# Optimization experiments

Hardware: AMD Instinct MI355X
Metric: run time of the kernel (lower is better)

Reference implementation:

```python
import jax, jax.numpy as jnp
import numpy as np

B, S, D = 16, 2048, 768
DOWNS = [16, 32, 64, 128]


def setup_inputs() -> dict:
    key = jax.random.key(0)
    ks = jax.random.split(key, 2 + 4 * len(DOWNS))
    inp = {
        "x": jax.random.normal(ks[0], (B, S, D), dtype=jnp.float32),
        "mask": jax.random.randint(ks[1], (B, S), 0, len(DOWNS), dtype=jnp.int64),
    }
    k = 2
    for i, ds in enumerate(DOWNS):
        inp[f"Wd{i}"] = jax.random.normal(ks[k], (D, ds), dtype=jnp.float32) * 0.02; k += 1
        inp[f"bd{i}"] = jax.random.normal(ks[k], (ds,), dtype=jnp.float32) * 0.02; k += 1
        inp[f"Wu{i}"] = jax.random.normal(ks[k], (ds, D), dtype=jnp.float32) * 0.02; k += 1
        inp[f"bu{i}"] = jax.random.normal(ks[k], (D,), dtype=jnp.float32) * 0.02; k += 1
    return inp


def reference(x, mask,
              Wd0, bd0, Wu0, bu0,
              Wd1, bd1, Wu1, bu1,
              Wd2, bd2, Wu2, bu2,
              Wd3, bd3, Wu3, bu3):
    # eval path, inference_level==0: all experts densely computed, then
    # per-token random mask selects one expert output (with residual) and sums.
    params = [(Wd0, bd0, Wu0, bu0), (Wd1, bd1, Wu1, bu1),
              (Wd2, bd2, Wu2, bu2), (Wd3, bd3, Wu3, bu3)]
    out = jnp.zeros_like(x)
    for i, (Wd, bd, Wu, bu) in enumerate(params):
        down = jax.nn.relu(jnp.einsum('bsd,dk->bsk', x, Wd) + bd)  # dropout is identity in eval
        up = jnp.einsum('bsk,kd->bsd', down, Wu) + bu + x          # residual add
        sel = (mask == i)[..., None].astype(x.dtype)               # [B,S,1]
        out = out + up * sel
    return out
```

## Files before the change

kernel.cpp:

```cpp
#include <hip/hip_runtime.h>
#include <hip/hip_bf16.h>

#define DIM 768
#define NTOK 32768
#define TTOK 16
#define NBLK 128
#define GRID_MAIN 1024

typedef __attribute__((ext_vector_type(8))) short short8;
typedef __attribute__((ext_vector_type(4))) float f32x4;

__device__ __forceinline__ unsigned short f2bf(float f) {
  union { float f; unsigned int u; } v; v.f = f;
  unsigned int u = v.u;
  return (unsigned short)((u + 0x7fffu + ((u >> 16) & 1u)) >> 16);
}
__device__ __forceinline__ float bf2f(unsigned short u) {
  union { unsigned int u; float f; } v; v.u = ((unsigned int)u) << 16; return v.f;
}

__global__ void hist_kernel(const int* __restrict__ mask, int* __restrict__ hist) {
  int tid = threadIdx.x, b = blockIdx.x;
  int gid = b * 256 + tid;
  int wv = tid >> 6, lane = tid & 63;
  int e = mask[gid] & 3;
  __shared__ int wcnt[4][4];
  #pragma unroll
  for (int q = 0; q < 4; ++q) {
    unsigned long long m = __ballot(e == q);
    if (lane == 0) wcnt[wv][q] = __popcll(m);
  }
  __syncthreads();
  if (tid < 4)
    hist[tid * NBLK + b] = wcnt[0][tid] + wcnt[1][tid] + wcnt[2][tid] + wcnt[3][tid];
}

__global__ void scan_kernel(const int* __restrict__ hist, int* __restrict__ base,
                            int* __restrict__ meta) {
  int lane = threadIdx.x;
  int v[8];
  int lsum = 0;
  #pragma unroll
  for (int j = 0; j < 8; ++j) {
    int t = hist[lane * 8 + j];
    v[j] = lsum; lsum += t;
  }
  int inc = lsum;
  #pragma unroll
  for (int d = 1; d < 64; d <<= 1) {
    int u = __shfl_up(inc, d);
    if (lane >= d) inc += u;
  }
  int excl = inc - lsum;
  #pragma unroll
  for (int j = 0; j < 8; ++j) base[lane * 8 + j] = excl + v[j];
  __syncthreads();
  if (lane == 0) {
    int est[5];
    #pragma unroll
    for (int e = 0; e < 4; ++e) est[e] = base[e * NBLK];
    est[4] = NTOK;
    int s = 0;
    #pragma unroll
    for (int e = 0; e < 5; ++e) meta[e] = est[e];
    #pragma unroll
    for (int e = 0; e < 4; ++e) {
      meta[8 + e] = s;
      s += (est[e + 1] - est[e] + TTOK - 1) / TTOK;
    }
    meta[12] = s;
  }
}

__global__ void scatter_kernel(const int* __restrict__ mask, const int* __restrict__ base,
                               int* __restrict__ lists) {
  int tid = threadIdx.x, b = blockIdx.x;
  int gid = b * 256 + tid;
  int wv = tid >> 6, lane = tid & 63;
  int e = mask[gid] & 3;
  __shared__ int wcnt[4][4];
  __shared__ int wbase[4][4];
  unsigned long long lt = (1ull << lane) - 1ull;
  int rank = 0;
  #pragma unroll
  for (int q = 0; q < 4; ++q) {
    unsigned long long m = __ballot(e == q);
    if (e == q) rank = __popcll(m & lt);
    if (lane == 0) wcnt[wv][q] = __popcll(m);
  }
  __syncthreads();
  if (tid < 4) {
    int s = 0;
    #pragma unroll
    for (int w2 = 0; w2 < 4; ++w2) { int c = wcnt[w2][tid]; wbase[w2][tid] = s; s += c; }
  }
  __syncthreads();
  lists[base[e * NBLK + b] + wbase[wv][e] + rank] = gid;
}

__global__ void prep_kernel(const float* __restrict__ Wd0, const float* __restrict__ Wd1,
                            const float* __restrict__ Wd2, const float* __restrict__ Wd3,
                            const float* __restrict__ Wu0, const float* __restrict__ Wu1,
                            const float* __restrict__ Wu2, const float* __restrict__ Wu3,
                            unsigned short* __restrict__ wdT, unsigned short* __restrict__ wuT) {
  int e = blockIdx.x;
  int ds = 16 << e;
  int lgK = (e == 0) ? 5 : (4 + e);
  int KP = 1 << lgK;
  const float* Wd = (e == 0) ? Wd0 : (e == 1) ? Wd1 : (e == 2) ? Wd2 : Wd3;
  const float* Wu = (e == 0) ? Wu0 : (e == 1) ? Wu1 : (e == 2) ? Wu2 : Wu3;
  const int WOFF[4] = {0, 12288, 36864, 86016};
  const int UOFF[4] = {0, 24576, 49152, 98304};
  int stride = gridDim.y * 256;
  int start = blockIdx.y * 256 + threadIdx.x;
  int nd = ds * DIM;
  for (int i = start; i < nd; i += stride) {
    int k = i / DIM, d = i - k * DIM;
    wdT[WOFF[e] + i] = f2bf(Wd[d * ds + k]);
  }
  int nu = DIM << lgK;
  for (int i = start; i < nu; i += stride) {
    int dc = i >> lgK, k = i & (KP - 1);
    wuT[UOFF[e] + i] = (k < ds) ? f2bf(Wu[k * DIM + dc]) : (unsigned short)0;
  }
}

struct Pref {
  float4 v[6];
  int tk[4];
};

__device__ __forceinline__ void issue_prefetch(
    int w, int wv, int lane,
    const int* __restrict__ meta, const int* __restrict__ lists,
    const float* __restrict__ x, Pref& p) {
  const int* ts = meta + 8;
  int e = (w >= ts[2]) ? ((w >= ts[3]) ? 3 : 2) : ((w >= ts[1]) ? 1 : 0);
  int base = (w - ts[e]) * TTOK;
  int cnt = meta[e + 1] - meta[e];
  const int* listsE = lists + meta[e];
  #pragma unroll
  for (int i = 0; i < 4; ++i) {
    int r = base + wv * 4 + i;
    p.tk[i] = (r < cnt) ? listsE[r] : -1;
  }
  #pragma unroll
  for (int i = 0; i < 2; ++i) {
    int t = p.tk[i];
    const float* src = x + (size_t)((t >= 0) ? t : 0) * DIM;
    #pragma unroll
    for (int j = 0; j < 3; ++j) {
      float4 vv = {0.f, 0.f, 0.f, 0.f};
      if (t >= 0) vv = *(const float4*)(src + j * 256 + lane * 4);
      p.v[i * 3 + j] = vv;
    }
  }
}

template <int E>
__device__ __forceinline__ void moe_tile(
    int wv, int lane, int tid,
    const float* __restrict__ x,
    const unsigned short* __restrict__ wdT, const unsigned short* __restrict__ wuT,
    const float* __restrict__ bd, const float* __restrict__ bu,
    float* __restrict__ out, const int mytk[4],
    unsigned short* xsol, float* dnpart, unsigned short (*dn)[136]) {
  constexpr int DS = 16 << E;
  constexpr int KP = (E == 0) ? 32 : DS;
  constexpr int NTA = DS / 16;
  constexpr int SPLIT_N = (NTA < 4) ? NTA : 4;
  constexpr int SPLIT_K = 4 / SPLIT_N;
  constexpr int NTB = NTA / SPLIT_N;
  constexpr int KLEN = DIM / SPLIT_K;
  constexpr int KB = KP / 32;
  constexpr int WOFF[4] = {0, 12288, 36864, 86016};
  constexpr int UOFF[4] = {0, 24576, 49152, 98304};
  const unsigned short* wd = wdT + WOFF[E];
  const unsigned short* wu = wuT + UOFF[E];
  #define XS(r) (xsol + (r) * 776)
  #define OL(r) (xsol + (r) * 772)

  int lrow = lane & 15, kg = lane >> 4;

  if (SPLIT_K > 1) {
    for (int i = tid; i < TTOK * DS; i += 256) dnpart[i] = 0.f;
  }
  __syncthreads();

  int nsub = wv % SPLIT_N, ksub = wv / SPLIT_N;
  int d_base = ksub * KLEN;

  f32x4 acc[NTB];
  #pragma unroll
  for (int nb = 0; nb < NTB; ++nb) acc[nb] = f32x4{0.f, 0.f, 0.f, 0.f};

  for (int d0 = 0; d0 < KLEN; d0 += 64) {
    #pragma unroll
    for (int u = 0; u < 2; ++u) {
      int d = d_base + d0 + u * 32;
      short8 a = *(const short8*)(XS(lrow) + d + kg * 8);
      #pragma unroll
      for (int nb = 0; nb < NTB; ++nb) {
        int n = nsub * NTB + nb;
        short8 b = *(const short8*)(wd + (size_t)(n * 16 + lrow) * DIM + d + kg * 8);
        acc[nb] = __builtin_amdgcn_mfma_f32_16x16x32_bf16(a, b, acc[nb], 0, 0, 0);
      }
    }
  }

  if (SPLIT_K > 1) {
    #pragma unroll
    for (int nb = 0; nb < NTB; ++nb) {
      int kc = (nsub * NTB + nb) * 16 + lrow;
      #pragma unroll
      for (int r = 0; r < 4; ++r)
        atomicAdd(&dnpart[(kg * 4 + r) * DS + kc], acc[nb][r]);
    }
    __syncthreads();
    for (int i = tid; i < TTOK * KP; i += 256) {
      int tt = i / KP, k = i - tt * KP;
      float v = (k < DS) ? fmaxf(dnpart[tt * DS + k] + bd[k], 0.f) : 0.f;
      dn[tt][k] = f2bf(v);
    }
  } else {
    #pragma unroll
    for (int nb = 0; nb < NTB; ++nb) {
      int kc = (nsub * NTB + nb) * 16 + lrow;
      float bv = bd[kc];
      #pragma unroll
      for (int r = 0; r < 4; ++r)
        dn[kg * 4 + r][kc] = f2bf(fmaxf(acc[nb][r] + bv, 0.f));
    }
  }
  __syncthreads();

  short8 afr[KB];
  #pragma unroll
  for (int k = 0; k < KB; ++k) afr[k] = *(const short8*)&dn[lrow][k * 32 + kg * 8];

  #pragma unroll 3
  for (int nn = 0; nn < 12; ++nn) {
    int n = wv * 12 + nn;
    f32x4 c = {0.f, 0.f, 0.f, 0.f};
    #pragma unroll
    for (int k = 0; k < KB; ++k) {
      short8 b = *(const short8*)(wu + (size_t)(n * 16 + lrow) * KP + k * 32 + kg * 8);
      c = __builtin_amdgcn_mfma_f32_16x16x32_bf16(afr[k], b, c, 0, 0, 0);
    }
    int dcol = n * 16 + lrow;
    float bv = bu[dcol];
    #pragma unroll
    for (int r = 0; r < 4; ++r)
      OL(kg * 4 + r)[dcol] = f2bf(c[r] + bv);
  }
  __syncthreads();

  #pragma unroll
  for (int i = 0; i < 4; ++i) {
    int r = wv * 4 + i;
    int t = mytk[i];
    if (t < 0) continue;
    const float* xsrc = x + (size_t)t * DIM;
    float* dst = out + (size_t)t * DIM;
    #pragma unroll
    for (int j = 0; j < 3; ++j) {
      int c = j * 256 + lane * 4;
      float4 xv = *(const float4*)(xsrc + c);
      ushort4 ub = *(const ushort4*)(OL(r) + c);
      float4 o;
      o.x = xv.x + bf2f(ub.x);
      o.y = xv.y + bf2f(ub.y);
      o.z = xv.z + bf2f(ub.z);
      o.w = xv.w + bf2f(ub.w);
      *(float4*)(dst + c) = o;
    }
  }
  __syncthreads();
  #undef XS
  #undef OL
}

__global__ __launch_bounds__(256, 4) void moe_main(
    const float* __restrict__ x,
    const int* __restrict__ meta, const int* __restrict__ lists,
    const unsigned short* __restrict__ wdT, const unsigned short* __restrict__ wuT,
    const float* __restrict__ bd0, const float* __restrict__ bd1,
    const float* __restrict__ bd2, const float* __restrict__ bd3,
    const float* __restrict__ bu0, const float* __restrict__ bu1,
    const float* __restrict__ bu2, const float* __restrict__ bu3,
    float* __restrict__ out) {
  __shared__ unsigned short xsol[TTOK * 776];
  __shared__ float dnpart[TTOK * 32];
  __shared__ unsigned short dn[TTOK][136];
  int tid = threadIdx.x, wv = tid >> 6, lane = tid & 63;
  const int* ts = meta + 8;
  int ntiles = ts[4];
  int w0 = blockIdx.x;
  if (w0 >= ntiles) return;

  Pref p;
  issue_prefetch(w0, wv, lane, meta, lists, x, p);

  for (int w = w0; w < ntiles; w += GRID_MAIN) {
    int t2 = p.tk[2], t3 = p.tk[3];
    float4 s[6];
    {
      const float* s2 = x + (size_t)((t2 >= 0) ? t2 : 0) * DIM;
      const float* s3 = x + (size_t)((t3 >= 0) ? t3 : 0) * DIM;
      #pragma unroll
      for (int j = 0; j < 3; ++j) {
        float4 a = {0.f, 0.f, 0.f, 0.f}, b = {0.f, 0.f, 0.f, 0.f};
        if (t2 >= 0) a = *(const float4*)(s2 + j * 256 + lane * 4);
        if (t3 >= 0) b = *(const float4*)(s3 + j * 256 + lane * 4);
        s[j] = a; s[3 + j] = b;
      }
    }
    #pragma unroll
    for (int i = 0; i < 2; ++i) {
      int r = wv * 4 + i;
      #pragma unroll
      for (int j = 0; j < 3; ++j) {
        float4 vv = p.v[i * 3 + j];
        ushort4 b;
        b.x = f2bf(vv.x); b.y = f2bf(vv.y); b.z = f2bf(vv.z); b.w = f2bf(vv.w);
        *(ushort4*)(xsol + r * 776 + j * 256 + lane * 4) = b;
      }
    }
    #pragma unroll
    for (int i = 0; i < 2; ++i) {
      int r = wv * 4 + 2 + i;
      #pragma unroll
      for (int j = 0; j < 3; ++j) {
        float4 vv = s[i * 3 + j];
        ushort4 b;
        b.x = f2bf(vv.x); b.y = f2bf(vv.y); b.z = f2bf(vv.z); b.w = f2bf(vv.w);
        *(ushort4*)(xsol + r * 776 + j * 256 + lane * 4) = b;
      }
    }
    int mytk[4];
    #pragma unroll
    for (int i = 0; i < 4; ++i) mytk[i] = p.tk[i];

    int wn = w + GRID_MAIN;
    if (wn < ntiles) issue_prefetch(wn, wv, lane, meta, lists, x, p);

    int e = (w >= ts[2]) ? ((w >= ts[3]) ? 3 : 2) : ((w >= ts[1]) ? 1 : 0);
    if (e == 0)
      moe_tile<0>(wv, lane, tid, x, wdT, wuT, bd0, bu0, out, mytk, xsol, dnpart, dn);
    else if (e == 1)
      moe_tile<1>(wv, lane, tid, x, wdT, wuT, bd1, bu1, out, mytk, xsol, dnpart, dn);
    else if (e == 2)
      moe_tile<2>(wv, lane, tid, x, wdT, wuT, bd2, bu2, out, mytk, xsol, dnpart, dn);
    else
      moe_tile<3>(wv, lane, tid, x, wdT, wuT, bd3, bu3, out, mytk, xsol, dnpart, dn);
  }
}

extern "C" void kernel_launch(void* const* d_in, const int* in_sizes, int n_in,
                              void* d_out, int out_size, void* d_ws, size_t ws_size,
                              hipStream_t stream) {
  const float* x = (const float*)d_in[0];
  const int* mask = (const int*)d_in[1];
  const float* Wd[4]; const float* bd[4]; const float* Wu[4]; const float* bu[4];
  for (int i = 0; i < 4; ++i) {
    Wd[i] = (const float*)d_in[2 + 4 * i];
    bd[i] = (const float*)d_in[3 + 4 * i];
    Wu[i] = (const float*)d_in[4 + 4 * i];
    bu[i] = (const float*)d_in[5 + 4 * i];
  }
  char* ws = (char*)d_ws;
  int* hist = (int*)ws;
  int* base = (int*)(ws + 2048);
  int* meta = (int*)(ws + 4096);
  int* lists = (int*)(ws + 4352);
  unsigned short* wdT = (unsigned short*)(ws + 135424);
  unsigned short* wuT = (unsigned short*)(ws + 504064);

  hist_kernel<<<NBLK, 256, 0, stream>>>(mask, hist);
  scan_kernel<<<1, 64, 0, stream>>>(hist, base, meta);
  scatter_kernel<<<NBLK, 256, 0, stream>>>(mask, base, lists);
  prep_kernel<<<dim3(4, 32), 256, 0, stream>>>(Wd[0], Wd[1], Wd[2], Wd[3],
                                               Wu[0], Wu[1], Wu[2], Wu[3], wdT, wuT);
  moe_main<<<GRID_MAIN, 256, 0, stream>>>(x, meta, lists, wdT, wuT,
                                          bd[0], bd[1], bd[2], bd[3],
                                          bu[0], bu[1], bu[2], bu[3],
                                          (float*)d_out);
}
```

Measured before the change: 96.68 us.

## Reuse LDS bf16 x copy for residual, prefetch all rows, stagger block starts

The residual add now reads the bf16 copy of x already staged in shared memory and fuses it into the up-projection epilogue. This removes the second global read of each x row in the output pass. The prefetch path now loads all four token rows for the next tile, and blocks are staggered with s_sleep by cohort. __syncthreads is replaced by an explicit lgkmcnt wait plus s_barrier. The cost is that the residual is now bf16-rounded and summed in bf16, which adds numerical error, and the larger prefetch needs more registers.

Result: no change. 96.83 us (+0.2%).

```diff
diff --git a/kernel.cpp b/kernel.cpp
--- a/kernel.cpp
+++ b/kernel.cpp
@@ -6,6 +6,7 @@
 #define TTOK 16
 #define NBLK 128
 #define GRID_MAIN 1024
+#define XP 772
 
 typedef __attribute__((ext_vector_type(8))) short short8;
 typedef __attribute__((ext_vector_type(4))) float f32x4;
@@ -17,6 +18,12 @@
 }
 __device__ __forceinline__ float bf2f(unsigned short u) {
   union { unsigned int u; float f; } v; v.u = ((unsigned int)u) << 16; return v.f;
+}
+
+__device__ __forceinline__ void barrier_lds() {
+  asm volatile("s_waitcnt lgkmcnt(0)" ::: "memory");
+  __builtin_amdgcn_s_barrier();
+  asm volatile("" ::: "memory");
 }
 
 __global__ void hist_kernel(const int* __restrict__ mask, int* __restrict__ hist) {
@@ -125,8 +132,12 @@
   }
 }
 
+__device__ __forceinline__ int expert_of(int w, const int* __restrict__ ts) {
+  return (w >= ts[2]) ? ((w >= ts[3]) ? 3 : 2) : ((w >= ts[1]) ? 1 : 0);
+}
+
 struct Pref {
-  float4 v[6];
+  float4 v[12];
   int tk[4];
 };
 
@@ -135,7 +146,7 @@
     const int* __restrict__ meta, const int* __restrict__ lists,
     const float* __restrict__ x, Pref& p) {
   const int* ts = meta + 8;
-  int e = (w >= ts[2]) ? ((w >= ts[3]) ? 3 : 2) : ((w >= ts[1]) ? 1 : 0);
+  int e = expert_of(w, ts);
   int base = (w - ts[e]) * TTOK;
   int cnt = meta[e + 1] - meta[e];
   const int* listsE = lists + meta[e];
@@ -145,7 +156,7 @@
     p.tk[i] = (r < cnt) ? listsE[r] : -1;
   }
   #pragma unroll
-  for (int i = 0; i < 2; ++i) {
+  for (int i = 0; i < 4; ++i) {
     int t = p.tk[i];
     const float* src = x + (size_t)((t >= 0) ? t : 0) * DIM;
     #pragma unroll
@@ -160,11 +171,11 @@
 template <int E>
 __device__ __forceinline__ void moe_tile(
     int wv, int lane, int tid,
-    const float* __restrict__ x,
     const unsigned short* __restrict__ wdT, const unsigned short* __restrict__ wuT,
     const float* __restrict__ bd, const float* __restrict__ bu,
     float* __restrict__ out, const int mytk[4],
-    unsigned short* xsol, float* dnpart, unsigned short (*dn)[136]) {
+    unsigned short* __restrict__ xsol, float* __restrict__ dnpart,
+    unsigned short (*dn)[136]) {
   constexpr int DS = 16 << E;
   constexpr int KP = (E == 0) ? 32 : DS;
   constexpr int NTA = DS / 16;
@@ -177,15 +188,13 @@
   constexpr int UOFF[4] = {0, 24576, 49152, 98304};
   const unsigned short* wd = wdT + WOFF[E];
   const unsigned short* wu = wuT + UOFF[E];
-  #define XS(r) (xsol + (r) * 776)
-  #define OL(r) (xsol + (r) * 772)
 
   int lrow = lane & 15, kg = lane >> 4;
 
   if (SPLIT_K > 1) {
     for (int i = tid; i < TTOK * DS; i += 256) dnpart[i] = 0.f;
   }
-  __syncthreads();
+  barrier_lds();
 
   int nsub = wv % SPLIT_N, ksub = wv / SPLIT_N;
   int d_base = ksub * KLEN;
@@ -198,7 +207,7 @@
     #pragma unroll
     for (int u = 0; u < 2; ++u) {
       int d = d_base + d0 + u * 32;
-      short8 a = *(const short8*)(XS(lrow) + d + kg * 8);
+      short8 a = *(const short8*)(xsol + lrow * XP + d + kg * 8);
       #pragma unroll
       for (int nb = 0; nb < NTB; ++nb) {
         int n = nsub * NTB + nb;
@@ -216,7 +225,7 @@
       for (int r = 0; r < 4; ++r)
         atomicAdd(&dnpart[(kg * 4 + r) * DS + kc], acc[nb][r]);
     }
-    __syncthreads();
+    barrier_lds();
     for (int i = tid; i < TTOK * KP; i += 256) {
       int tt = i / KP, k = i - tt * KP;
       float v = (k < DS) ? fmaxf(dnpart[tt * DS + k] + bd[k], 0.f) : 0.f;
@@ -232,7 +241,7 @@
         dn[kg * 4 + r][kc] = f2bf(fmaxf(acc[nb][r] + bv, 0.f));
     }
   }
-  __syncthreads();
+  barrier_lds();
 
   short8 afr[KB];
   #pragma unroll
@@ -250,34 +259,31 @@
     int dcol = n * 16 + lrow;
     float bv = bu[dcol];
     #pragma unroll
-    for (int r = 0; r < 4; ++r)
-      OL(kg * 4 + r)[dcol] = f2bf(c[r] + bv);
-  }
-  __syncthreads();
+    for (int r = 0; r < 4; ++r) {
+      int t = kg * 4 + r;
+      unsigned short* cell = xsol + t * XP + dcol;
+      float xr = bf2f(*cell);
+      *cell = f2bf(c[r] + bv + xr);
+    }
+  }
+  barrier_lds();
 
   #pragma unroll
   for (int i = 0; i < 4; ++i) {
     int r = wv * 4 + i;
     int t = mytk[i];
     if (t < 0) continue;
-    const float* xsrc = x + (size_t)t * DIM;
     float* dst = out + (size_t)t * DIM;
     #pragma unroll
     for (int j = 0; j < 3; ++j) {
       int c = j * 256 + lane * 4;
-      float4 xv = *(const float4*)(xsrc + c);
-      ushort4 ub = *(const ushort4*)(OL(r) + c);
+      ushort4 ub = *(const ushort4*)(xsol + r * XP + c);
       float4 o;
-      o.x = xv.x + bf2f(ub.x);
-      o.y = xv.y + bf2f(ub.y);
-      o.z = xv.z + bf2f(ub.z);
-      o.w = xv.w + bf2f(ub.w);
+      o.x = bf2f(ub.x); o.y = bf2f(ub.y); o.z = bf2f(ub.z); o.w = bf2f(ub.w);
       *(float4*)(dst + c) = o;
     }
   }
-  __syncthreads();
-  #undef XS
-  #undef OL
+  barrier_lds();
 }
 
 __global__ __launch_bounds__(256, 4) void moe_main(
@@ -289,52 +295,31 @@
     const float* __restrict__ bu0, const float* __restrict__ bu1,
     const float* __restrict__ bu2, const float* __restrict__ bu3,
     float* __restrict__ out) {
-  __shared__ unsigned short xsol[TTOK * 776];
+  __shared__ unsigned short xsol[TTOK * XP];
   __shared__ float dnpart[TTOK * 32];
   __shared__ unsigned short dn[TTOK][136];
   int tid = threadIdx.x, wv = tid >> 6, lane = tid & 63;
   const int* ts = meta + 8;
   int ntiles = ts[4];
-  int w0 = blockIdx.x;
-  if (w0 >= ntiles) return;
+  int w = blockIdx.x;
+  if (w >= ntiles) return;
 
   Pref p;
-  issue_prefetch(w0, wv, lane, meta, lists, x, p);
-
-  for (int w = w0; w < ntiles; w += GRID_MAIN) {
-    int t2 = p.tk[2], t3 = p.tk[3];
-    float4 s[6];
-    {
-      const float* s2 = x + (size_t)((t2 >= 0) ? t2 : 0) * DIM;
-      const float* s3 = x + (size_t)((t3 >= 0) ? t3 : 0) * DIM;
-      #pragma unroll
-      for (int j = 0; j < 3; ++j) {
-        float4 a = {0.f, 0.f, 0.f, 0.f}, b = {0.f, 0.f, 0.f, 0.f};
-        if (t2 >= 0) a = *(const float4*)(s2 + j * 256 + lane * 4);
-        if (t3 >= 0) b = *(const float4*)(s3 + j * 256 + lane * 4);
-        s[j] = a; s[3 + j] = b;
-      }
-    }
-    #pragma unroll
-    for (int i = 0; i < 2; ++i) {
+  issue_prefetch(w, wv, lane, meta, lists, x, p);
+
+  int cohort = blockIdx.x >> 8;
+  for (int i = 0; i < cohort; ++i) __builtin_amdgcn_s_sleep(64);
+
+  for (; w < ntiles; w += GRID_MAIN) {
+    #pragma unroll
+    for (int i = 0; i < 4; ++i) {
       int r = wv * 4 + i;
       #pragma unroll
       for (int j = 0; j < 3; ++j) {
         float4 vv = p.v[i * 3 + j];
         ushort4 b;
         b.x = f2bf(vv.x); b.y = f2bf(vv.y); b.z = f2bf(vv.z); b.w = f2bf(vv.w);
-        *(ushort4*)(xsol + r * 776 + j * 256 + lane * 4) = b;
-      }
-    }
-    #pragma unroll
-    for (int i = 0; i < 2; ++i) {
-      int r = wv * 4 + 2 + i;
-      #pragma unroll
-      for (int j = 0; j < 3; ++j) {
-        float4 vv = s[i * 3 + j];
-        ushort4 b;
-        b.x = f2bf(vv.x); b.y = f2bf(vv.y); b.z = f2bf(vv.z); b.w = f2bf(vv.w);
-        *(ushort4*)(xsol + r * 776 + j * 256 + lane * 4) = b;
+        *(ushort4*)(xsol + r * XP + j * 256 + lane * 4) = b;
       }
     }
     int mytk[4];
@@ -344,15 +329,15 @@
     int wn = w + GRID_MAIN;
     if (wn < ntiles) issue_prefetch(wn, wv, lane, meta, lists, x, p);
 
-    int e = (w >= ts[2]) ? ((w >= ts[3]) ? 3 : 2) : ((w >= ts[1]) ? 1 : 0);
+    int e = expert_of(w, ts);
     if (e == 0)
-      moe_tile<0>(wv, lane, tid, x, wdT, wuT, bd0, bu0, out, mytk, xsol, dnpart, dn);
+      moe_tile<0>(wv, lane, tid, wdT, wuT, bd0, bu0, out, mytk, xsol, dnpart, dn);
     else if (e == 1)
-      moe_tile<1>(wv, lane, tid, x, wdT, wuT, bd1, bu1, out, mytk, xsol, dnpart, dn);
+      moe_tile<1>(wv, lane, tid, wdT, wuT, bd1, bu1, out, mytk, xsol, dnpart, dn);
     else if (e == 2)
-      moe_tile<2>(wv, lane, tid, x, wdT, wuT, bd2, bu2, out, mytk, xsol, dnpart, dn);
+      moe_tile<2>(wv, lane, tid, wdT, wuT, bd2, bu2, out, mytk, xsol, dnpart, dn);
     else
-      moe_tile<3>(wv, lane, tid, x, wdT, wuT, bd3, bu3, out, mytk, xsol, dnpart, dn);
+      moe_tile<3>(wv, lane, tid, wdT, wuT, bd3, bu3, out, mytk, xsol, dnpart, dn);
   }
 }
 
```

## Stage token rows into LDS via async global-to-LDS copies in fp32

Applied to the files above, without the earlier changes.

The per-token x rows are now copied straight from global memory into a float LDS buffer with global_load_lds, which drops the register-held software prefetch of the next tile and the bf16 conversion on store. Conversion to bf16 now happens when each MFMA A-fragment is read from LDS. The grid is halved to 512 blocks and launch bounds are lowered to 2 blocks per SM, since the fp32 staging buffer doubles LDS use. The cost is that next-tile loads no longer overlap the current tile's compute, A-fragment LDS reads are wider, and occupancy is lower.

After: 104.5 us. +8.1%, slower.

```diff
diff --git a/kernel.cpp b/kernel.cpp
--- a/kernel.cpp
+++ b/kernel.cpp
@@ -5,7 +5,8 @@
 #define NTOK 32768
 #define TTOK 16
 #define NBLK 128
-#define GRID_MAIN 1024
+#define GRID_MAIN 512
+#define XPITCH 772
 
 typedef __attribute__((ext_vector_type(8))) short short8;
 typedef __attribute__((ext_vector_type(4))) float f32x4;
@@ -17,6 +18,20 @@
 }
 __device__ __forceinline__ float bf2f(unsigned short u) {
   union { unsigned int u; float f; } v; v.u = ((unsigned int)u) << 16; return v.f;
+}
+__device__ __forceinline__ short8 f2bf8(float4 lo, float4 hi) {
+  short8 r;
+  r[0] = (short)f2bf(lo.x); r[1] = (short)f2bf(lo.y);
+  r[2] = (short)f2bf(lo.z); r[3] = (short)f2bf(lo.w);
+  r[4] = (short)f2bf(hi.x); r[5] = (short)f2bf(hi.y);
+  r[6] = (short)f2bf(hi.z); r[7] = (short)f2bf(hi.w);
+  return r;
+}
+
+__device__ __forceinline__ void async_cp16(const void* g, void* l) {
+  __builtin_amdgcn_global_load_lds(
+      (const __attribute__((address_space(1))) unsigned int*)g,
+      (__attribute__((address_space(3))) unsigned int*)l, 16, 0, 0);
 }
 
 __global__ void hist_kernel(const int* __restrict__ mask, int* __restrict__ hist) {
@@ -125,36 +140,8 @@
   }
 }
 
-struct Pref {
-  float4 v[6];
-  int tk[4];
-};
-
-__device__ __forceinline__ void issue_prefetch(
-    int w, int wv, int lane,
-    const int* __restrict__ meta, const int* __restrict__ lists,
-    const float* __restrict__ x, Pref& p) {
-  const int* ts = meta + 8;
-  int e = (w >= ts[2]) ? ((w >= ts[3]) ? 3 : 2) : ((w >= ts[1]) ? 1 : 0);
-  int base = (w - ts[e]) * TTOK;
-  int cnt = meta[e + 1] - meta[e];
-  const int* listsE = lists + meta[e];
-  #pragma unroll
-  for (int i = 0; i < 4; ++i) {
-    int r = base + wv * 4 + i;
-    p.tk[i] = (r < cnt) ? listsE[r] : -1;
-  }
-  #pragma unroll
-  for (int i = 0; i < 2; ++i) {
-    int t = p.tk[i];
-    const float* src = x + (size_t)((t >= 0) ? t : 0) * DIM;
-    #pragma unroll
-    for (int j = 0; j < 3; ++j) {
-      float4 vv = {0.f, 0.f, 0.f, 0.f};
-      if (t >= 0) vv = *(const float4*)(src + j * 256 + lane * 4);
-      p.v[i * 3 + j] = vv;
-    }
-  }
+__device__ __forceinline__ int expert_of(int w, const int* __restrict__ ts) {
+  return (w >= ts[2]) ? ((w >= ts[3]) ? 3 : 2) : ((w >= ts[1]) ? 1 : 0);
 }
 
 template <int E>
@@ -164,7 +151,7 @@
     const unsigned short* __restrict__ wdT, const unsigned short* __restrict__ wuT,
     const float* __restrict__ bd, const float* __restrict__ bu,
     float* __restrict__ out, const int mytk[4],
-    unsigned short* xsol, float* dnpart, unsigned short (*dn)[136]) {
+    float* xsf, float* dnpart, unsigned short (*dn)[136]) {
   constexpr int DS = 16 << E;
   constexpr int KP = (E == 0) ? 32 : DS;
   constexpr int NTA = DS / 16;
@@ -177,8 +164,7 @@
   constexpr int UOFF[4] = {0, 24576, 49152, 98304};
   const unsigned short* wd = wdT + WOFF[E];
   const unsigned short* wu = wuT + UOFF[E];
-  #define XS(r) (xsol + (r) * 776)
-  #define OL(r) (xsol + (r) * 772)
+  #define OL(r) (((unsigned short*)xsf) + (r) * 772)
 
   int lrow = lane & 15, kg = lane >> 4;
 
@@ -198,7 +184,8 @@
     #pragma unroll
     for (int u = 0; u < 2; ++u) {
       int d = d_base + d0 + u * 32;
-      short8 a = *(const short8*)(XS(lrow) + d + kg * 8);
+      const float* ap = xsf + lrow * XPITCH + d + kg * 8;
+      short8 a = f2bf8(*(const float4*)ap, *(const float4*)(ap + 4));
       #pragma unroll
       for (int nb = 0; nb < NTB; ++nb) {
         int n = nsub * NTB + nb;
@@ -276,11 +263,10 @@
     }
   }
   __syncthreads();
-  #undef XS
   #undef OL
 }
 
-__global__ __launch_bounds__(256, 4) void moe_main(
+__global__ __launch_bounds__(256, 2) void moe_main(
     const float* __restrict__ x,
     const int* __restrict__ meta, const int* __restrict__ lists,
     const unsigned short* __restrict__ wdT, const unsigned short* __restrict__ wuT,
@@ -289,70 +275,45 @@
     const float* __restrict__ bu0, const float* __restrict__ bu1,
     const float* __restrict__ bu2, const float* __restrict__ bu3,
     float* __restrict__ out) {
-  __shared__ unsigned short xsol[TTOK * 776];
+  __shared__ float xsf[TTOK * XPITCH];
   __shared__ float dnpart[TTOK * 32];
   __shared__ unsigned short dn[TTOK][136];
   int tid = threadIdx.x, wv = tid >> 6, lane = tid & 63;
   const int* ts = meta + 8;
   int ntiles = ts[4];
-  int w0 = blockIdx.x;
-  if (w0 >= ntiles) return;
-
-  Pref p;
-  issue_prefetch(w0, wv, lane, meta, lists, x, p);
-
-  for (int w = w0; w < ntiles; w += GRID_MAIN) {
-    int t2 = p.tk[2], t3 = p.tk[3];
-    float4 s[6];
-    {
-      const float* s2 = x + (size_t)((t2 >= 0) ? t2 : 0) * DIM;
-      const float* s3 = x + (size_t)((t3 >= 0) ? t3 : 0) * DIM;
-      #pragma unroll
-      for (int j = 0; j < 3; ++j) {
-        float4 a = {0.f, 0.f, 0.f, 0.f}, b = {0.f, 0.f, 0.f, 0.f};
-        if (t2 >= 0) a = *(const float4*)(s2 + j * 256 + lane * 4);
-        if (t3 >= 0) b = *(const float4*)(s3 + j * 256 + lane * 4);
-        s[j] = a; s[3 + j] = b;
+
+  for (int w = blockIdx.x; w < ntiles; w += GRID_MAIN) {
+    int e = expert_of(w, ts);
+    int base = (w - ts[e]) * TTOK;
+    int cnt = meta[e + 1] - meta[e];
+    const int* listsE = lists + meta[e];
+
+    int mytk[4];
+    #pragma unroll
+    for (int i = 0; i < 4; ++i) {
+      int r = base + wv * 4 + i;
+      mytk[i] = (r < cnt) ? listsE[r] : -1;
+    }
+    #pragma unroll
+    for (int i = 0; i < 4; ++i) {
+      int t = mytk[i];
+      if (t >= 0) {
+        const float* src = x + (size_t)t * DIM + lane * 4;
+        float* dstb = xsf + (size_t)(wv * 4 + i) * XPITCH;
+        #pragma unroll
+        for (int j = 0; j < 3; ++j)
+          async_cp16(src + j * 256, dstb + j * 256);
       }
     }
-    #pragma unroll
-    for (int i = 0; i < 2; ++i) {
-      int r = wv * 4 + i;
-      #pragma unroll
-      for (int j = 0; j < 3; ++j) {
-        float4 vv = p.v[i * 3 + j];
-        ushort4 b;
-        b.x = f2bf(vv.x); b.y = f2bf(vv.y); b.z = f2bf(vv.z); b.w = f2bf(vv.w);
-        *(ushort4*)(xsol + r * 776 + j * 256 + lane * 4) = b;
-      }
-    }
-    #pragma unroll
-    for (int i = 0; i < 2; ++i) {
-      int r = wv * 4 + 2 + i;
-      #pragma unroll
-      for (int j = 0; j < 3; ++j) {
-        float4 vv = s[i * 3 + j];
-        ushort4 b;
-        b.x = f2bf(vv.x); b.y = f2bf(vv.y); b.z = f2bf(vv.z); b.w = f2bf(vv.w);
-        *(ushort4*)(xsol + r * 776 + j * 256 + lane * 4) = b;
-      }
-    }
-    int mytk[4];
-    #pragma unroll
-    for (int i = 0; i < 4; ++i) mytk[i] = p.tk[i];
-
-    int wn = w + GRID_MAIN;
-    if (wn < ntiles) issue_prefetch(wn, wv, lane, meta, lists, x, p);
-
-    int e = (w >= ts[2]) ? ((w >= ts[3]) ? 3 : 2) : ((w >= ts[1]) ? 1 : 0);
+
     if (e == 0)
-      moe_tile<0>(wv, lane, tid, x, wdT, wuT, bd0, bu0, out, mytk, xsol, dnpart, dn);
+      moe_tile<0>(wv, lane, tid, x, wdT, wuT, bd0, bu0, out, mytk, xsf, dnpart, dn);
     else if (e == 1)
-      moe_tile<1>(wv, lane, tid, x, wdT, wuT, bd1, bu1, out, mytk, xsol, dnpart, dn);
+      moe_tile<1>(wv, lane, tid, x, wdT, wuT, bd1, bu1, out, mytk, xsf, dnpart, dn);
     else if (e == 2)
-      moe_tile<2>(wv, lane, tid, x, wdT, wuT, bd2, bu2, out, mytk, xsol, dnpart, dn);
+      moe_tile<2>(wv, lane, tid, x, wdT, wuT, bd2, bu2, out, mytk, xsf, dnpart, dn);
     else
-      moe_tile<3>(wv, lane, tid, x, wdT, wuT, bd3, bu3, out, mytk, xsol, dnpart, dn);
+      moe_tile<3>(wv, lane, tid, x, wdT, wuT, bd3, bu3, out, mytk, xsf, dnpart, dn);
   }
 }
 
```
